# Kernel optimization log

Hardware: AMD Instinct MI355X
Metric: run time of the kernel (lower is better)

Reference implementation:

```python
import jax, jax.numpy as jnp
import numpy as np

B, N, C = 4, 8192, 256
E = 262144
OUT = 256  # out_ch * heads = 128 * 2


def setup_inputs() -> dict:
    key = jax.random.key(0)
    ks = jax.random.split(key, 6)
    x = jax.random.normal(ks[0], (B, N, C), dtype=jnp.float32)
    edge_index = jax.random.randint(ks[1], (2, E), 0, N, dtype=jnp.int64)
    s = 1.0 / np.sqrt(C)
    W_self = jax.random.normal(ks[2], (C, OUT), dtype=jnp.float32) * s
    b_self = jax.random.normal(ks[3], (OUT,), dtype=jnp.float32) * 0.01
    W_neigh = jax.random.normal(ks[4], (C, OUT), dtype=jnp.float32) * s
    b_neigh = jax.random.normal(ks[5], (OUT,), dtype=jnp.float32) * 0.01
    return {"x": x, "edge_index": edge_index, "W_self": W_self, "b_self": b_self,
            "W_neigh": W_neigh, "b_neigh": b_neigh}


def _build_A_hat(edge_index, n):
    # A[i,j] = multiplicity of edge (src=i, dst=j), plus self loops (identity),
    # matching torch.sparse_coo_tensor(...).to_dense() which sums duplicates.
    src, dst = edge_index[0], edge_index[1]
    A = jnp.zeros((n, n), dtype=jnp.float32).at[src, dst].add(1.0)
    A = A + jnp.eye(n, dtype=jnp.float32)
    deg = jnp.clip(A.sum(axis=1), 1.0, None)  # [N]
    return A / deg[:, None]  # row-normalized adjacency


def reference(x, edge_index, W_self, b_self, W_neigh, b_neigh):
    n = x.shape[1]
    A_hat = _build_A_hat(edge_index, n)            # [N, N]
    h_self = x @ W_self + b_self                   # [B, N, OUT]
    y = jnp.einsum('ij,bjc->bic', A_hat, x)        # neighbor aggregation
    h_nei = y @ W_neigh + b_neigh                  # [B, N, OUT]
    return jax.nn.gelu(h_self + h_nei, approximate=False)
```

## Files before the change

### kernel.cpp

```cpp
#include <hip/hip_runtime.h>
#include <math.h>

#define BB 4
#define NN 8192
#define CC 256
#define OUTC 256
#define EE 262144
#define MROWS (BB*NN)
#define CAP 96

typedef __attribute__((ext_vector_type(8))) short short8;
typedef __attribute__((ext_vector_type(4))) short s16x4;
typedef __attribute__((ext_vector_type(4))) float f32x4;

__device__ inline unsigned short f2bf(float f) {
    union { float f; unsigned u; } a; a.f = f;
    unsigned u = a.u;
    u += 0x7fffu + ((u >> 16) & 1u);
    return (unsigned short)(u >> 16);
}
__device__ inline float bf2f(unsigned short h) {
    union { unsigned u; float f; } a; a.u = ((unsigned)h) << 16;
    return a.f;
}
__device__ inline float gelu1(float v) {
    float t = v * (0.7978845608f + 0.0356774081f * v * v);
    float e = __expf(2.0f * t);
    float th = 1.0f - 2.0f / (e + 1.0f);
    return 0.5f * v * (1.0f + th);
}


__global__ __launch_bounds__(256) void prep_w(const float* __restrict__ Ws,
                                              const float* __restrict__ Wn,
                                              unsigned short* __restrict__ Wt2,
                                              int* __restrict__ cnt) {
    int bi = blockIdx.x;
    int tid = threadIdx.x;
    if (bi >= 32) {
        cnt[(bi - 32) * 256 + tid] = 0;
        return;
    }
    __shared__ float tile[64][65];
    int kt = bi >> 3, nt = bi & 7;
    int k0 = kt * 64, n0 = nt * 64;
    const float* W = (n0 < 256) ? Ws : Wn;
    int ncol = n0 & 255;
#pragma unroll
    for (int p = 0; p < 4; p++) {
        int krow = p * 16 + (tid >> 4);
        int col = (tid & 15) * 4;
        float4 v = *(const float4*)&W[(size_t)(k0 + krow) * 256 + ncol + col];
        tile[krow][col + 0] = v.x;
        tile[krow][col + 1] = v.y;
        tile[krow][col + 2] = v.z;
        tile[krow][col + 3] = v.w;
    }
    __syncthreads();
#pragma unroll
    for (int e = 0; e < 2; e++) {
        int idx = e * 256 + tid;
        int lane = idx & 63;
        int ni = (idx >> 6) & 3;
        int kkl = idx >> 8;
        int kk = kt * 2 + kkl;
        int qrow = lane >> 4, fr = lane & 15;
        short8 t;
#pragma unroll
        for (int j = 0; j < 8; j++)
            t[j] = (short)f2bf(tile[kkl * 32 + qrow * 8 + j][ni * 16 + fr]);
        *(short8*)&Wt2[(size_t)(((nt * 8 + kk) * 4 + ni) * 512) + lane * 8] = t;
    }
}


#define APAD 8
#define ALD (256 + APAD)

__global__ __launch_bounds__(256, 2) void gemm_fill(const float* __restrict__ X,
                                                    const unsigned short* __restrict__ Wt2,
                                                    unsigned short* __restrict__ Zb,
                                                    unsigned short* __restrict__ U,
                                                    const int* __restrict__ ei,
                                                    int* __restrict__ cnt,
                                                    unsigned short* __restrict__ adjb) {
    __shared__ unsigned short sA[64 * ALD];
    int bi = blockIdx.x;
    int tid = threadIdx.x;

    if (bi >= 512) {
        int e = (bi - 512) * 256 + tid;
        for (; e < EE; e += 256 * 256) {
            int s = ei[e] & (NN - 1);
            int d = ei[EE + e] & (NN - 1);
            int slot = atomicAdd(&cnt[s], 1);
            if (slot < CAP) adjb[(size_t)s * CAP + slot] = (unsigned short)d;
        }
        return;
    }

    int wave = tid >> 6, lane = tid & 63;
    int row0 = bi * 64;
    int qrow = lane >> 4;
    int fr = lane & 15;

#pragma unroll
    for (int q = 0; q < 16; q++) {
        int f = q * 1024 + tid * 4;
        int rr = f >> 8, k0 = f & 255;
        float4 v = *(const float4*)&X[(size_t)(row0 + rr) * 256 + k0];
        s16x4 t;
        t[0] = (short)f2bf(v.x); t[1] = (short)f2bf(v.y);
        t[2] = (short)f2bf(v.z); t[3] = (short)f2bf(v.w);
        *(s16x4*)&sA[rr * ALD + k0] = t;
    }
    __syncthreads();

#pragma unroll 1
    for (int sp = 0; sp < 2; sp++) {
        int colbase = wave * 128 + sp * 64;
        int ct = wave * 2 + sp;
        const unsigned short* Bp = Wt2 + (size_t)ct * 8 * 4 * 512 + lane * 8;

        f32x4 acc[4][4];
#pragma unroll
        for (int ni = 0; ni < 4; ni++)
#pragma unroll
            for (int mi = 0; mi < 4; mi++) acc[ni][mi] = (f32x4)0.0f;

        short8 bbuf[3][4];
#pragma unroll
        for (int ni = 0; ni < 4; ni++) {
            bbuf[0][ni] = *(const short8*)&Bp[(size_t)(0 * 4 + ni) * 512];
            bbuf[1][ni] = *(const short8*)&Bp[(size_t)(1 * 4 + ni) * 512];
        }

#pragma unroll
        for (int kk = 0; kk < 8; kk++) {
            if (kk < 6) {
#pragma unroll
                for (int ni = 0; ni < 4; ni++)
                    bbuf[(kk + 2) % 3][ni] =
                        *(const short8*)&Bp[(size_t)((kk + 2) * 4 + ni) * 512];
            }
            int ak = kk * 32 + qrow * 8;
            short8 af[4];
#pragma unroll
            for (int mi = 0; mi < 4; mi++)
                af[mi] = *(const short8*)&sA[(mi * 16 + fr) * ALD + ak];
#pragma unroll
            for (int ni = 0; ni < 4; ni++)
#pragma unroll
                for (int mi = 0; mi < 4; mi++)
                    acc[ni][mi] = __builtin_amdgcn_mfma_f32_16x16x32_bf16(
                        bbuf[kk % 3][ni], af[mi], acc[ni][mi], 0, 0, 0);
        }

#pragma unroll
        for (int mi = 0; mi < 4; mi++) {
            size_t row = (size_t)(row0 + mi * 16 + fr);
#pragma unroll
            for (int ni = 0; ni < 4; ni++) {
                int col = colbase + ni * 16 + qrow * 4;
                s16x4 t;
                t[0] = (short)f2bf(acc[ni][mi][0]);
                t[1] = (short)f2bf(acc[ni][mi][1]);
                t[2] = (short)f2bf(acc[ni][mi][2]);
                t[3] = (short)f2bf(acc[ni][mi][3]);
                if (colbase < 256) *(s16x4*)&Zb[row * 512 + 256 + col] = t;
                else               *(s16x4*)&U[row * 256 + (col - 256)] = t;
            }
        }
    }
}


__global__ __launch_bounds__(256) void agg_gelu(const unsigned short* __restrict__ U,
                                                const int* __restrict__ cnt,
                                                const unsigned short* __restrict__ adjb,
                                                const float* __restrict__ bs,
                                                const float* __restrict__ bn,
                                                float* __restrict__ Out) {
    int r = blockIdx.x & 7;
    int q = blockIdx.x >> 3;
    int b = r & 3;
    int g = ((r >> 2) << 10) + q;
    int i = (g << 2) + (threadIdx.x >> 6);
    int lane = threadIdx.x & 63;
    int c = lane * 4;

    const unsigned short* Urow = U + (size_t)b * NN * 256 + c;
    size_t row = (size_t)b * NN + i;

    const unsigned* ZbP = (const unsigned*)Out;
    unsigned zl = __builtin_nontemporal_load(&ZbP[row * 256 + 128 + (c >> 1)]);
    unsigned zh = __builtin_nontemporal_load(&ZbP[row * 256 + 128 + (c >> 1) + 1]);
    float z0 = bf2f((unsigned short)(zl & 0xffff));
    float z1 = bf2f((unsigned short)(zl >> 16));
    float z2 = bf2f((unsigned short)(zh & 0xffff));
    float z3 = bf2f((unsigned short)(zh >> 16));
    float4 vs = *(const float4*)&bs[c];
    float4 vn = *(const float4*)&bn[c];

    ushort4 sv = *(const ushort4*)&Urow[(size_t)i * 256];
    float a0 = bf2f(sv.x), a1 = bf2f(sv.y), a2 = bf2f(sv.z), a3 = bf2f(sv.w);

    int deg = cnt[i];
    float s = 1.0f / (float)(1 + deg);
    int m = min(deg, CAP);
    const unsigned short* lst = &adjb[(size_t)i * CAP];
    const unsigned* lp = (const unsigned*)lst;

    int p = 0;
    for (; p + 16 <= m; p += 16) {
        unsigned w[8];
#pragma unroll
        for (int t = 0; t < 8; t++) w[t] = lp[(p >> 1) + t];
        ushort4 v[16];
#pragma unroll
        for (int t = 0; t < 8; t++) {
            int j0 = w[t] & 0xffff;
            int j1 = w[t] >> 16;
            v[2 * t + 0] = *(const ushort4*)&Urow[(size_t)j0 * 256];
            v[2 * t + 1] = *(const ushort4*)&Urow[(size_t)j1 * 256];
        }
#pragma unroll
        for (int t = 0; t < 16; t++) {
            a0 += bf2f(v[t].x); a1 += bf2f(v[t].y);
            a2 += bf2f(v[t].z); a3 += bf2f(v[t].w);
        }
    }
    for (; p + 4 <= m; p += 4) {
        ushort4 v[4];
#pragma unroll
        for (int t = 0; t < 4; t++) {
            int j = lst[p + t];
            v[t] = *(const ushort4*)&Urow[(size_t)j * 256];
        }
#pragma unroll
        for (int t = 0; t < 4; t++) {
            a0 += bf2f(v[t].x); a1 += bf2f(v[t].y);
            a2 += bf2f(v[t].z); a3 += bf2f(v[t].w);
        }
    }
    for (; p < m; p++) {
        int j = lst[p];
        ushort4 v = *(const ushort4*)&Urow[(size_t)j * 256];
        a0 += bf2f(v.x); a1 += bf2f(v.y); a2 += bf2f(v.z); a3 += bf2f(v.w);
    }

    float v0 = z0 + vs.x + vn.x + s * a0;
    float v1 = z1 + vs.y + vn.y + s * a1;
    float v2 = z2 + vs.z + vn.z + s * a2;
    float v3 = z3 + vs.w + vn.w + s * a3;

    f32x4 gout;
    gout[0] = gelu1(v0);
    gout[1] = gelu1(v1);
    gout[2] = gelu1(v2);
    gout[3] = gelu1(v3);
    __builtin_nontemporal_store(gout, (f32x4*)&Out[row * 256 + c]);
}


extern "C" void kernel_launch(void* const* d_in, const int* in_sizes, int n_in,
                              void* d_out, int out_size, void* d_ws, size_t ws_size,
                              hipStream_t stream) {
    const float* x   = (const float*)d_in[0];
    const int* ei    = (const int*)d_in[1];
    const float* Ws  = (const float*)d_in[2];
    const float* bsv = (const float*)d_in[3];
    const float* Wn  = (const float*)d_in[4];
    const float* bnv = (const float*)d_in[5];
    float* out = (float*)d_out;

    char* ws = (char*)d_ws;
    size_t o = 0;
    unsigned short* U   = (unsigned short*)(ws + o); o += (size_t)MROWS * OUTC * 2;
    unsigned short* Wt2 = (unsigned short*)(ws + o); o += (size_t)512 * 256 * 2;
    int* cnt = (int*)(ws + o);  o += (size_t)NN * 4;
    unsigned short* adjb = (unsigned short*)(ws + o); o += (size_t)NN * CAP * 2;

    prep_w<<<64, 256, 0, stream>>>(Ws, Wn, Wt2, cnt);

    gemm_fill<<<768, 256, 0, stream>>>(x, Wt2, (unsigned short*)out, U, ei, cnt, adjb);

    agg_gelu<<<8192, 256, 0, stream>>>(U, cnt, adjb, bsv, bnv, out);
}
```

Measured before the change: 158.6 us.

## Fuse prep, GEMM/fill and aggregation into one cooperative kernel with grid syncs

```diff
diff --git a/kernel.cpp b/kernel.cpp
--- a/kernel.cpp
+++ b/kernel.cpp
@@ -1,13 +1,16 @@
 #include <hip/hip_runtime.h>
+#include <hip/hip_cooperative_groups.h>
 #include <math.h>
 
-#define BB 4
+namespace cg = cooperative_groups;
+
 #define NN 8192
-#define CC 256
-#define OUTC 256
 #define EE 262144
-#define MROWS (BB*NN)
+#define MROWS 32768
 #define CAP 96
+#define APAD 8
+#define ALD (256 + APAD)
+#define SH_BYTES (64 * ALD * 2)
 
 typedef __attribute__((ext_vector_type(8))) short short8;
 typedef __attribute__((ext_vector_type(4))) short s16x4;
@@ -31,17 +34,11 @@
 }
 
 
-__global__ __launch_bounds__(256) void prep_w(const float* __restrict__ Ws,
-                                              const float* __restrict__ Wn,
-                                              unsigned short* __restrict__ Wt2,
-                                              int* __restrict__ cnt) {
-    int bi = blockIdx.x;
-    int tid = threadIdx.x;
-    if (bi >= 32) {
-        cnt[(bi - 32) * 256 + tid] = 0;
-        return;
-    }
-    __shared__ float tile[64][65];
+__device__ inline void do_prep(int bi, int tid, char* shmem,
+                               const float* __restrict__ Ws, const float* __restrict__ Wn,
+                               unsigned short* __restrict__ Wt2, int* __restrict__ cnt) {
+    if (bi >= 32) { cnt[(bi - 32) * 256 + tid] = 0; return; }
+    float (*tile)[65] = (float (*)[65])shmem;
     int kt = bi >> 3, nt = bi & 7;
     int k0 = kt * 64, n0 = nt * 64;
     const float* W = (n0 < 256) ? Ws : Wn;
@@ -60,49 +57,35 @@
 #pragma unroll
     for (int e = 0; e < 2; e++) {
         int idx = e * 256 + tid;
-        int lane = idx & 63;
+        int l2 = idx & 63;
         int ni = (idx >> 6) & 3;
         int kkl = idx >> 8;
         int kk = kt * 2 + kkl;
-        int qrow = lane >> 4, fr = lane & 15;
+        int qr = l2 >> 4, fr2 = l2 & 15;
         short8 t;
 #pragma unroll
         for (int j = 0; j < 8; j++)
-            t[j] = (short)f2bf(tile[kkl * 32 + qrow * 8 + j][ni * 16 + fr]);
-        *(short8*)&Wt2[(size_t)(((nt * 8 + kk) * 4 + ni) * 512) + lane * 8] = t;
-    }
-}
-
-
-#define APAD 8
-#define ALD (256 + APAD)
-
-__global__ __launch_bounds__(256, 2) void gemm_fill(const float* __restrict__ X,
-                                                    const unsigned short* __restrict__ Wt2,
-                                                    unsigned short* __restrict__ Zb,
-                                                    unsigned short* __restrict__ U,
-                                                    const int* __restrict__ ei,
-                                                    int* __restrict__ cnt,
-                                                    unsigned short* __restrict__ adjb) {
-    __shared__ unsigned short sA[64 * ALD];
-    int bi = blockIdx.x;
-    int tid = threadIdx.x;
-
-    if (bi >= 512) {
-        int e = (bi - 512) * 256 + tid;
-        for (; e < EE; e += 256 * 256) {
-            int s = ei[e] & (NN - 1);
-            int d = ei[EE + e] & (NN - 1);
-            int slot = atomicAdd(&cnt[s], 1);
-            if (slot < CAP) adjb[(size_t)s * CAP + slot] = (unsigned short)d;
-        }
-        return;
-    }
-
+            t[j] = (short)f2bf(tile[kkl * 32 + qr * 8 + j][ni * 16 + fr2]);
+        *(short8*)&Wt2[(size_t)(((nt * 8 + kk) * 4 + ni) * 512) + l2 * 8] = t;
+    }
+}
+
+__device__ inline void do_fill(int e, const int* __restrict__ ei,
+                               int* __restrict__ cnt, unsigned short* __restrict__ adjb) {
+    int s = ei[e] & (NN - 1);
+    int d = ei[EE + e] & (NN - 1);
+    int slot = atomicAdd(&cnt[s], 1);
+    if (slot < CAP) adjb[(size_t)s * CAP + slot] = (unsigned short)d;
+}
+
+__device__ inline void do_gemm(int bi, int tid, unsigned short* sA,
+                               const float* __restrict__ X,
+                               const unsigned short* __restrict__ Wt2,
+                               unsigned short* __restrict__ Zb,
+                               unsigned short* __restrict__ U) {
     int wave = tid >> 6, lane = tid & 63;
     int row0 = bi * 64;
-    int qrow = lane >> 4;
-    int fr = lane & 15;
+    int qrow = lane >> 4, fr = lane & 15;
 
 #pragma unroll
     for (int q = 0; q < 16; q++) {
@@ -120,7 +103,7 @@
     for (int sp = 0; sp < 2; sp++) {
         int colbase = wave * 128 + sp * 64;
         int ct = wave * 2 + sp;
-        const unsigned short* Bp = Wt2 + (size_t)ct * 8 * 4 * 512 + lane * 8;
+        const unsigned short* Bp = Wt2 + (size_t)ct * 16384 + lane * 8;
 
         f32x4 acc[4][4];
 #pragma unroll
@@ -134,7 +117,6 @@
             bbuf[0][ni] = *(const short8*)&Bp[(size_t)(0 * 4 + ni) * 512];
             bbuf[1][ni] = *(const short8*)&Bp[(size_t)(1 * 4 + ni) * 512];
         }
-
 #pragma unroll
         for (int kk = 0; kk < 8; kk++) {
             if (kk < 6) {
@@ -155,7 +137,6 @@
                     acc[ni][mi] = __builtin_amdgcn_mfma_f32_16x16x32_bf16(
                         bbuf[kk % 3][ni], af[mi], acc[ni][mi], 0, 0, 0);
         }
-
 #pragma unroll
         for (int mi = 0; mi < 4; mi++) {
             size_t row = (size_t)(row0 + mi * 16 + fr);
@@ -174,24 +155,12 @@
     }
 }
 
-
-__global__ __launch_bounds__(256) void agg_gelu(const unsigned short* __restrict__ U,
-                                                const int* __restrict__ cnt,
-                                                const unsigned short* __restrict__ adjb,
-                                                const float* __restrict__ bs,
-                                                const float* __restrict__ bn,
-                                                float* __restrict__ Out) {
-    int r = blockIdx.x & 7;
-    int q = blockIdx.x >> 3;
-    int b = r & 3;
-    int g = ((r >> 2) << 10) + q;
-    int i = (g << 2) + (threadIdx.x >> 6);
-    int lane = threadIdx.x & 63;
-    int c = lane * 4;
-
-    const unsigned short* Urow = U + (size_t)b * NN * 256 + c;
+__device__ inline void agg_node(int i, int b, int c,
+                                const unsigned short* __restrict__ Ubase,
+                                const int* __restrict__ cnt,
+                                const unsigned short* __restrict__ adjb,
+                                float4 vs, float4 vn, float* __restrict__ Out) {
     size_t row = (size_t)b * NN + i;
-
     const unsigned* ZbP = (const unsigned*)Out;
     unsigned zl = __builtin_nontemporal_load(&ZbP[row * 256 + 128 + (c >> 1)]);
     unsigned zh = __builtin_nontemporal_load(&ZbP[row * 256 + 128 + (c >> 1) + 1]);
@@ -199,10 +168,8 @@
     float z1 = bf2f((unsigned short)(zl >> 16));
     float z2 = bf2f((unsigned short)(zh & 0xffff));
     float z3 = bf2f((unsigned short)(zh >> 16));
-    float4 vs = *(const float4*)&bs[c];
-    float4 vn = *(const float4*)&bn[c];
-
-    ushort4 sv = *(const ushort4*)&Urow[(size_t)i * 256];
+
+    ushort4 sv = *(const ushort4*)&Ubase[(size_t)i * 256];
     float a0 = bf2f(sv.x), a1 = bf2f(sv.y), a2 = bf2f(sv.z), a3 = bf2f(sv.w);
 
     int deg = cnt[i];
@@ -221,8 +188,8 @@
         for (int t = 0; t < 8; t++) {
             int j0 = w[t] & 0xffff;
             int j1 = w[t] >> 16;
-            v[2 * t + 0] = *(const ushort4*)&Urow[(size_t)j0 * 256];
-            v[2 * t + 1] = *(const ushort4*)&Urow[(size_t)j1 * 256];
+            v[2 * t + 0] = *(const ushort4*)&Ubase[(size_t)j0 * 256];
+            v[2 * t + 1] = *(const ushort4*)&Ubase[(size_t)j1 * 256];
         }
 #pragma unroll
         for (int t = 0; t < 16; t++) {
@@ -235,7 +202,7 @@
 #pragma unroll
         for (int t = 0; t < 4; t++) {
             int j = lst[p + t];
-            v[t] = *(const ushort4*)&Urow[(size_t)j * 256];
+            v[t] = *(const ushort4*)&Ubase[(size_t)j * 256];
         }
 #pragma unroll
         for (int t = 0; t < 4; t++) {
@@ -245,7 +212,7 @@
     }
     for (; p < m; p++) {
         int j = lst[p];
-        ushort4 v = *(const ushort4*)&Urow[(size_t)j * 256];
+        ushort4 v = *(const ushort4*)&Ubase[(size_t)j * 256];
         a0 += bf2f(v.x); a1 += bf2f(v.y); a2 += bf2f(v.z); a3 += bf2f(v.w);
     }
 
@@ -260,6 +227,89 @@
     gout[2] = gelu1(v2);
     gout[3] = gelu1(v3);
     __builtin_nontemporal_store(gout, (f32x4*)&Out[row * 256 + c]);
+}
+
+
+__global__ __launch_bounds__(256, 2) void fused(
+        const float* __restrict__ X, const int* __restrict__ ei,
+        const float* __restrict__ Ws, const float* __restrict__ bs,
+        const float* __restrict__ Wn, const float* __restrict__ bn,
+        float* __restrict__ Out,
+        unsigned short* __restrict__ U, unsigned short* __restrict__ Wt2,
+        int* __restrict__ cnt, unsigned short* __restrict__ adjb) {
+    __shared__ __align__(16) char shmem[SH_BYTES];
+    int bi = blockIdx.x;
+    int tid = threadIdx.x;
+    cg::grid_group grid = cg::this_grid();
+
+    if (bi < 64) do_prep(bi, tid, shmem, Ws, Wn, Wt2, cnt);
+    grid.sync();
+
+    {
+        int e = bi * 256 + tid;
+        do_fill(e, ei, cnt, adjb);
+        do_fill(e + 131072, ei, cnt, adjb);
+    }
+    do_gemm(bi, tid, (unsigned short*)shmem, X, Wt2, (unsigned short*)Out, U);
+    grid.sync();
+
+    {
+        int wave = tid >> 6, lane = tid & 63, c = lane * 4;
+        int r = bi & 7;
+        int b = r & 3, h = r >> 2;
+        int blk = bi >> 3;
+        const unsigned short* Ubase = U + (size_t)b * NN * 256 + c;
+        float4 vs = *(const float4*)&bs[c];
+        float4 vn = *(const float4*)&bn[c];
+        int ibase = h * 4096 + (blk * 4 + wave) * 16;
+#pragma unroll 1
+        for (int k = 0; k < 16; k++)
+            agg_node(ibase + k, b, c, Ubase, cnt, adjb, vs, vn, Out);
+    }
+}
+
+
+__global__ __launch_bounds__(256) void prep_w_k(const float* __restrict__ Ws,
+                                                const float* __restrict__ Wn,
+                                                unsigned short* __restrict__ Wt2,
+                                                int* __restrict__ cnt) {
+    __shared__ __align__(16) char shmem[64 * 65 * 4];
+    do_prep(blockIdx.x, threadIdx.x, shmem, Ws, Wn, Wt2, cnt);
+}
+
+__global__ __launch_bounds__(256, 2) void gemm_fill_k(const float* __restrict__ X,
+                                                      const unsigned short* __restrict__ Wt2,
+                                                      unsigned short* __restrict__ Zb,
+                                                      unsigned short* __restrict__ U,
+                                                      const int* __restrict__ ei,
+                                                      int* __restrict__ cnt,
+                                                      unsigned short* __restrict__ adjb) {
+    __shared__ __align__(16) char shmem[SH_BYTES];
+    int bi = blockIdx.x;
+    if (bi >= 512) {
+        for (int e = (bi - 512) * 256 + threadIdx.x; e < EE; e += 256 * 256)
+            do_fill(e, ei, cnt, adjb);
+        return;
+    }
+    do_gemm(bi, threadIdx.x, (unsigned short*)shmem, X, Wt2, Zb, U);
+}
+
+__global__ __launch_bounds__(256) void agg_k(const unsigned short* __restrict__ U,
+                                             const int* __restrict__ cnt,
+                                             const unsigned short* __restrict__ adjb,
+                                             const float* __restrict__ bs,
+                                             const float* __restrict__ bn,
+                                             float* __restrict__ Out) {
+    int r = blockIdx.x & 7;
+    int q = blockIdx.x >> 3;
+    int b = r & 3;
+    int g = ((r >> 2) << 10) + q;
+    int i = (g << 2) + (threadIdx.x >> 6);
+    int c = (threadIdx.x & 63) * 4;
+    const unsigned short* Ubase = U + (size_t)b * NN * 256 + c;
+    float4 vs = *(const float4*)&bs[c];
+    float4 vn = *(const float4*)&bn[c];
+    agg_node(i, b, c, Ubase, cnt, adjb, vs, vn, Out);
 }
 
 
@@ -276,14 +326,19 @@
 
     char* ws = (char*)d_ws;
     size_t o = 0;
-    unsigned short* U   = (unsigned short*)(ws + o); o += (size_t)MROWS * OUTC * 2;
+    unsigned short* U   = (unsigned short*)(ws + o); o += (size_t)MROWS * 256 * 2;
     unsigned short* Wt2 = (unsigned short*)(ws + o); o += (size_t)512 * 256 * 2;
     int* cnt = (int*)(ws + o);  o += (size_t)NN * 4;
     unsigned short* adjb = (unsigned short*)(ws + o); o += (size_t)NN * CAP * 2;
 
-    prep_w<<<64, 256, 0, stream>>>(Ws, Wn, Wt2, cnt);
-
-    gemm_fill<<<768, 256, 0, stream>>>(x, Wt2, (unsigned short*)out, U, ei, cnt, adjb);
-
-    agg_gelu<<<8192, 256, 0, stream>>>(U, cnt, adjb, bsv, bnv, out);
-}
+    void* args[] = { (void*)&x, (void*)&ei, (void*)&Ws, (void*)&bsv,
+                     (void*)&Wn, (void*)&bnv, (void*)&out,
+                     (void*)&U, (void*)&Wt2, (void*)&cnt, (void*)&adjb };
+    hipError_t err = hipLaunchCooperativeKernel((const void*)fused, dim3(512), dim3(256),
+                                                args, 0, stream);
+    if (err != hipSuccess) {
+        prep_w_k<<<64, 256, 0, stream>>>(Ws, Wn, Wt2, cnt);
+        gemm_fill_k<<<768, 256, 0, stream>>>(x, Wt2, (unsigned short*)out, U, ei, cnt, adjb);
+        agg_k<<<8192, 256, 0, stream>>>(U, cnt, adjb, bsv, bnv, out);
+    }
+}
```

Measured after the change: 339.3 us. 114% more time.
